# Kernel tuning notes

Hardware: AMD Instinct MI355X
Metric: run time of the kernel (lower is better)

Reference implementation:

```python
import jax, jax.numpy as jnp
import numpy as np

B, D, C = 16384, 2048, 1000  # batch, in_features (feature dim), out_features (classes)
INIT_SCALE = 10.0
EPS = 1e-12


def setup_inputs() -> dict:
    key = jax.random.key(0)
    k1, k2 = jax.random.split(key)
    x = jax.random.normal(k1, (B, D), dtype=jnp.float32)
    weights = jax.random.normal(k2, (C, D), dtype=jnp.float32)  # prototypes
    scales = jnp.ones((1,), dtype=jnp.float32) * INIT_SCALE
    return {"x": x, "weights": weights, "scales": scales}


def reference(x, weights, scales):
    # Pairwise Euclidean distance between features [B,D] and prototypes [C,D]
    x2 = jnp.sum(x * x, axis=-1, keepdims=True)            # [B,1]
    w2 = jnp.sum(weights * weights, axis=-1)               # [C]
    cross = jnp.einsum('bd,cd->bc', x, weights)            # [B,C]
    d2 = jnp.maximum(x2 + w2[None, :] - 2.0 * cross, EPS)  # clamp for sqrt stability
    distances = jnp.sqrt(d2)                               # [B,C]
    logits = -scales * distances  # dml forward: -self.learn(distances)
    return logits
```

## Files before the change

### kernel.cpp

```cpp
#include <hip/hip_runtime.h>
#include <hip/hip_bf16.h>
#include <stdint.h>

#define B_ROWS 16384
#define D_K    2048
#define C_COLS 1000
#define C_PAD  1024
#define EPS_D2 1e-12f

#define BM 256
#define BN 256
#define BK 32
#define NT (D_K / BK)
#define BUF_BYTES 32768
#define NBUF 4

typedef __attribute__((ext_vector_type(8))) short bf16x8;
typedef __attribute__((ext_vector_type(4))) float f32x4;

__device__ __forceinline__ void async16(void* lds, const void* g) {
    __builtin_amdgcn_global_load_lds(
        (const __attribute__((address_space(1))) unsigned int*)g,
        (__attribute__((address_space(3))) unsigned int*)lds,
        16, 0, 0);
}

__device__ __forceinline__ uint2 pack_bf16x4(float4 v) {
    union { __hip_bfloat162 h; uint32_t u; } a, b;
    a.h = __float22bfloat162_rn(make_float2(v.x, v.y));
    b.h = __float22bfloat162_rn(make_float2(v.z, v.w));
    uint2 r; r.x = a.u; r.y = b.u; return r;
}

__global__ __launch_bounds__(256) void prep_all(
    const float* __restrict__ x, const float* __restrict__ w,
    __hip_bfloat16* __restrict__ xb, __hip_bfloat16* __restrict__ wb,
    float* __restrict__ x2, float* __restrict__ w2) {
    const int t = threadIdx.x;
    const int wave = t >> 6;
    const int lane = t & 63;
    const int row = blockIdx.x * 4 + wave;

    const float* src;
    uint4* dst;
    float* norm_out;
    bool valid;
    if (row < B_ROWS) {
        src = x + (size_t)row * D_K;
        dst = (uint4*)(xb + (size_t)row * D_K);
        norm_out = x2 + row;
        valid = true;
    } else {
        int c = row - B_ROWS;
        src = w + (size_t)c * D_K;
        dst = (uint4*)(wb + (size_t)c * D_K);
        norm_out = w2 + c;
        valid = (c < C_COLS);
    }

    float4 v[8];
    if (valid) {
        const float4* s4 = (const float4*)src;
        #pragma unroll
        for (int i = 0; i < 4; i++) {
            v[2 * i]     = s4[2 * lane + 128 * i];
            v[2 * i + 1] = s4[2 * lane + 1 + 128 * i];
        }
    } else {
        #pragma unroll
        for (int i = 0; i < 8; i++) v[i] = make_float4(0.f, 0.f, 0.f, 0.f);
    }

    float ss = 0.f;
    #pragma unroll
    for (int i = 0; i < 8; i++)
        ss += v[i].x * v[i].x + v[i].y * v[i].y + v[i].z * v[i].z + v[i].w * v[i].w;

    #pragma unroll
    for (int i = 0; i < 4; i++) {
        uint2 a = pack_bf16x4(v[2 * i]);
        uint2 b = pack_bf16x4(v[2 * i + 1]);
        uint4 p; p.x = a.x; p.y = a.y; p.z = b.x; p.w = b.y;
        dst[lane + 64 * i] = p;
    }

    #pragma unroll
    for (int off = 32; off > 0; off >>= 1) ss += __shfl_down(ss, off, 64);
    if (lane == 0 && valid) *norm_out = ss;
}

__global__ __launch_bounds__(512, 2) void dml_gemm(
    const __hip_bfloat16* __restrict__ A,
    const __hip_bfloat16* __restrict__ Bm,
    const float* __restrict__ x2, const float* __restrict__ w2,
    const float* __restrict__ scales, float* __restrict__ out)
{
    __shared__ __align__(16) char smem[NBUF * BUF_BYTES];

    const int tid  = threadIdx.x;
    const int wave = tid >> 6;
    const int lane = tid & 63;
    const int wm = wave >> 2;
    const int wn = wave & 3;

    const int id  = blockIdx.x;
    const int xcd = id & 7;
    const int j5  = id >> 3;
    const int m0  = (xcd * 8 + (j5 & 7)) * BM;
    const int n0  = (j5 >> 3) * BN;

    const int L0 = tid, L1 = tid + 512;
    const int r0 = L0 >> 2, g0 = (L0 & 3) ^ ((r0 >> 1) & 3);
    const int r1 = L1 >> 2, g1 = (L1 & 3) ^ ((r1 >> 1) & 3);
    const __hip_bfloat16* pA0 = A  + (size_t)(m0 + r0) * D_K + g0 * 8;
    const __hip_bfloat16* pA1 = A  + (size_t)(m0 + r1) * D_K + g1 * 8;
    const __hip_bfloat16* pB0 = Bm + (size_t)(n0 + r0) * D_K + g0 * 8;
    const __hip_bfloat16* pB1 = Bm + (size_t)(n0 + r1) * D_K + g1 * 8;
    char* ldA0 = smem + L0 * 16;
    char* ldA1 = smem + L1 * 16;
    char* ldB0 = smem + 16384 + L0 * 16;
    char* ldB1 = smem + 16384 + L1 * 16;

    const int fr = lane & 15;
    const int fq = lane >> 4;
    const int ksw = (fq ^ ((fr >> 1) & 3)) * 16;
    const char* fA = smem + (wm * 128 + fr) * 64 + ksw;
    const char* fB = smem + 16384 + (wn * 64 + fr) * 64 + ksw;

    f32x4 acc[8][4] = {};

    #pragma unroll
    for (int tgt = 0; tgt < 3; ++tgt) {
        const int sbo = tgt * BUF_BYTES;
        async16(ldA0 + sbo, pA0 + tgt * BK);
        async16(ldA1 + sbo, pA1 + tgt * BK);
        async16(ldB0 + sbo, pB0 + tgt * BK);
        async16(ldB1 + sbo, pB1 + tgt * BK);
    }
    asm volatile("s_waitcnt vmcnt(8)" ::: "memory");
    __builtin_amdgcn_s_barrier();
    __builtin_amdgcn_sched_barrier(0);

    #pragma unroll 1
    for (int t = 0; t < NT; ++t) {
        const int bo  = (t & 3) * BUF_BYTES;
        const int tgt = t + 3;
        const bool do_stage = (tgt < NT);
        const int sbo = (tgt & 3) * BUF_BYTES;

        if (do_stage) {
            async16(ldA0 + sbo, pA0 + tgt * BK);
            async16(ldA1 + sbo, pA1 + tgt * BK);
        }
        bf16x8 b[4], a[4];
        #pragma unroll
        for (int q = 0; q < 4; ++q) b[q] = *(const bf16x8*)(fB + bo + q * 1024);
        #pragma unroll
        for (int i = 0; i < 4; ++i) a[i] = *(const bf16x8*)(fA + bo + i * 1024);
        __builtin_amdgcn_s_setprio(1);
        #pragma unroll
        for (int i = 0; i < 4; ++i)
            #pragma unroll
            for (int q = 0; q < 4; ++q)
                acc[i][q] = __builtin_amdgcn_mfma_f32_16x16x32_bf16(a[i], b[q], acc[i][q], 0, 0, 0);
        __builtin_amdgcn_s_setprio(0);

        if (do_stage) {
            async16(ldB0 + sbo, pB0 + tgt * BK);
            async16(ldB1 + sbo, pB1 + tgt * BK);
        }
        #pragma unroll
        for (int i = 0; i < 4; ++i) a[i] = *(const bf16x8*)(fA + bo + (4 + i) * 1024);
        __builtin_amdgcn_s_setprio(1);
        #pragma unroll
        for (int i = 0; i < 4; ++i)
            #pragma unroll
            for (int q = 0; q < 4; ++q)
                acc[4 + i][q] = __builtin_amdgcn_mfma_f32_16x16x32_bf16(a[i], b[q], acc[4 + i][q], 0, 0, 0);
        __builtin_amdgcn_s_setprio(0);

        if (t < NT - 3)      asm volatile("s_waitcnt vmcnt(8)" ::: "memory");
        else if (t == NT - 3) asm volatile("s_waitcnt vmcnt(4)" ::: "memory");
        else if (t == NT - 2) asm volatile("s_waitcnt vmcnt(0)" ::: "memory");
        if (t < NT - 1) {
            __builtin_amdgcn_s_barrier();
            __builtin_amdgcn_sched_barrier(0);
        }
    }

    const float s = scales[0];
    const int colb = n0 + wn * 64 + fr;
    const int rowb = m0 + wm * 128 + fq * 4;

    float w2v[4];
    #pragma unroll
    for (int q = 0; q < 4; ++q) w2v[q] = w2[colb + q * 16];

    #pragma unroll
    for (int i = 0; i < 8; ++i) {
        float x2v[4];
        #pragma unroll
        for (int r = 0; r < 4; ++r) x2v[r] = x2[rowb + i * 16 + r];
        #pragma unroll
        for (int q = 0; q < 4; ++q) {
            if (colb + q * 16 < C_COLS) {
                float* orow = out + (size_t)(rowb + i * 16) * C_COLS + colb + q * 16;
                #pragma unroll
                for (int r = 0; r < 4; ++r) {
                    float d2 = x2v[r] + w2v[q] - 2.0f * acc[i][q][r];
                    d2 = fmaxf(d2, EPS_D2);
                    orow[(size_t)r * C_COLS] = -s * __builtin_sqrtf(d2);
                }
            }
        }
    }
}

extern "C" void kernel_launch(void* const* d_in, const int* in_sizes, int n_in,
                              void* d_out, int out_size, void* d_ws, size_t ws_size,
                              hipStream_t stream) {
    const float* x      = (const float*)d_in[0];
    const float* w      = (const float*)d_in[1];
    const float* scales = (const float*)d_in[2];
    float* out = (float*)d_out;

    char* ws = (char*)d_ws;
    __hip_bfloat16* xb = (__hip_bfloat16*)ws;
    __hip_bfloat16* wb = (__hip_bfloat16*)(ws + (size_t)B_ROWS * D_K * 2);
    float* x2 = (float*)(ws + (size_t)B_ROWS * D_K * 2 + (size_t)C_PAD * D_K * 2);
    float* w2 = x2 + B_ROWS;

    prep_all<<<dim3((B_ROWS + C_PAD) / 4), dim3(256), 0, stream>>>(x, w, xb, wb, x2, w2);
    dml_gemm<<<dim3((B_ROWS / BM) * (C_PAD / BN)), dim3(512), 0, stream>>>(xb, wb, x2, w2, scales, out);
}
```

Measured before the change: 286.7 us.

## Software-pipeline LDS fragment loads one k-tile ahead of MFMA compute

The main loop now reads the next k-tile's A and B fragments from LDS into registers while the second half of the current tile's MFMAs run, instead of loading fragments right before they are used. The barrier moves to mid-iteration, and the global-to-LDS async loads for a tile are issued together after it, with vmcnt waits adjusted to match. The goal is to hide LDS read latency behind matrix-core work. The cost is extra live VGPRs for the double-buffered fragments, which could cause spills or lower occupancy under the 512-thread, 2-block launch bounds.

```diff
diff --git a/kernel.cpp b/kernel.cpp
--- a/kernel.cpp
+++ b/kernel.cpp
@@ -141,50 +141,65 @@
     __builtin_amdgcn_s_barrier();
     __builtin_amdgcn_sched_barrier(0);
 
+    bf16x8 aA[4], bb[4], a1[4];
+    #pragma unroll
+    for (int i = 0; i < 4; ++i) aA[i] = *(const bf16x8*)(fA + i * 1024);
+    #pragma unroll
+    for (int q = 0; q < 4; ++q) bb[q] = *(const bf16x8*)(fB + q * 1024);
+    #pragma unroll
+    for (int i = 0; i < 4; ++i) a1[i] = *(const bf16x8*)(fA + (4 + i) * 1024);
+
     #pragma unroll 1
     for (int t = 0; t < NT; ++t) {
-        const int bo  = (t & 3) * BUF_BYTES;
+        const int bo1 = ((t + 1) & 3) * BUF_BYTES;
         const int tgt = t + 3;
-        const bool do_stage = (tgt < NT);
-        const int sbo = (tgt & 3) * BUF_BYTES;
-
-        if (do_stage) {
-            async16(ldA0 + sbo, pA0 + tgt * BK);
-            async16(ldA1 + sbo, pA1 + tgt * BK);
-        }
-        bf16x8 b[4], a[4];
-        #pragma unroll
-        for (int q = 0; q < 4; ++q) b[q] = *(const bf16x8*)(fB + bo + q * 1024);
-        #pragma unroll
-        for (int i = 0; i < 4; ++i) a[i] = *(const bf16x8*)(fA + bo + i * 1024);
+
         __builtin_amdgcn_s_setprio(1);
         #pragma unroll
         for (int i = 0; i < 4; ++i)
             #pragma unroll
             for (int q = 0; q < 4; ++q)
-                acc[i][q] = __builtin_amdgcn_mfma_f32_16x16x32_bf16(a[i], b[q], acc[i][q], 0, 0, 0);
+                acc[i][q] = __builtin_amdgcn_mfma_f32_16x16x32_bf16(aA[i], bb[q], acc[i][q], 0, 0, 0);
         __builtin_amdgcn_s_setprio(0);
 
-        if (do_stage) {
-            async16(ldB0 + sbo, pB0 + tgt * BK);
-            async16(ldB1 + sbo, pB1 + tgt * BK);
-        }
-        #pragma unroll
-        for (int i = 0; i < 4; ++i) a[i] = *(const bf16x8*)(fA + bo + (4 + i) * 1024);
-        __builtin_amdgcn_s_setprio(1);
-        #pragma unroll
-        for (int i = 0; i < 4; ++i)
-            #pragma unroll
-            for (int q = 0; q < 4; ++q)
-                acc[4 + i][q] = __builtin_amdgcn_mfma_f32_16x16x32_bf16(a[i], b[q], acc[4 + i][q], 0, 0, 0);
-        __builtin_amdgcn_s_setprio(0);
-
-        if (t < NT - 3)      asm volatile("s_waitcnt vmcnt(8)" ::: "memory");
-        else if (t == NT - 3) asm volatile("s_waitcnt vmcnt(4)" ::: "memory");
+        if (t < NT - 2)       asm volatile("s_waitcnt vmcnt(4)" ::: "memory");
         else if (t == NT - 2) asm volatile("s_waitcnt vmcnt(0)" ::: "memory");
         if (t < NT - 1) {
             __builtin_amdgcn_s_barrier();
             __builtin_amdgcn_sched_barrier(0);
+        }
+
+        if (tgt < NT) {
+            const int sbo = (tgt & 3) * BUF_BYTES;
+            async16(ldA0 + sbo, pA0 + tgt * BK);
+            async16(ldA1 + sbo, pA1 + tgt * BK);
+            async16(ldB0 + sbo, pB0 + tgt * BK);
+            async16(ldB1 + sbo, pB1 + tgt * BK);
+        }
+
+        bf16x8 aN[4], bN[4];
+        if (t + 1 < NT) {
+            #pragma unroll
+            for (int i = 0; i < 4; ++i) aN[i] = *(const bf16x8*)(fA + bo1 + i * 1024);
+            #pragma unroll
+            for (int q = 0; q < 4; ++q) bN[q] = *(const bf16x8*)(fB + bo1 + q * 1024);
+        }
+
+        __builtin_amdgcn_s_setprio(1);
+        #pragma unroll
+        for (int i = 0; i < 4; ++i)
+            #pragma unroll
+            for (int q = 0; q < 4; ++q)
+                acc[4 + i][q] = __builtin_amdgcn_mfma_f32_16x16x32_bf16(a1[i], bb[q], acc[4 + i][q], 0, 0, 0);
+        __builtin_amdgcn_s_setprio(0);
+
+        if (t + 1 < NT) {
+            #pragma unroll
+            for (int i = 0; i < 4; ++i) a1[i] = *(const bf16x8*)(fA + bo1 + (4 + i) * 1024);
+            #pragma unroll
+            for (int i = 0; i < 4; ++i) aA[i] = aN[i];
+            #pragma unroll
+            for (int q = 0; q < 4; ++q) bb[q] = bN[q];
         }
     }
 
```

After: 287.9 us. No clear change (+0.4%).

## Restructure GEMM main loop into fine-grained 8-phase pipelined schedule

Applied to the files above, without the earlier changes.

Replaces the 4-buffer BK=32 loop with a 128-K-wide iteration split into eight phases over two 64-K buffers of two 32-K halves each. Async global-to-LDS loads are interleaved with LDS reads and MFMA blocks, with a barrier before and after each MFMA block. The aim is to spread memory issue evenly across compute and keep MFMAs fed. The cost is many more barriers per K step, a larger 128KB LDS footprint, and a fragile hand-tuned vmcnt accounting.

```diff
diff --git a/kernel.cpp b/kernel.cpp
--- a/kernel.cpp
+++ b/kernel.cpp
@@ -10,10 +10,7 @@
 
 #define BM 256
 #define BN 256
-#define BK 32
-#define NT (D_K / BK)
-#define BUF_BYTES 32768
-#define NBUF 4
+#define NIT (D_K / 128)
 
 typedef __attribute__((ext_vector_type(8))) short bf16x8;
 typedef __attribute__((ext_vector_type(4))) float f32x4;
@@ -89,13 +86,51 @@
     if (lane == 0 && valid) *norm_out = ss;
 }
 
+#define SLOT(buf, kh) ((buf) * 65536 + (kh) * 16384)
+
+#define SA(buf, kh, t) { \
+    async16(lA0 + SLOT(buf, kh), gA0 + (t) * 64 + (kh) * 32); \
+    async16(lA1 + SLOT(buf, kh), gA1 + (t) * 64 + (kh) * 32); }
+
+#define SB(buf, kh, t) { \
+    async16(lB0 + SLOT(buf, kh), gB0 + (t) * 64 + (kh) * 32); \
+    async16(lB1 + SLOT(buf, kh), gB1 + (t) * 64 + (kh) * 32); }
+
+#define RD_B(buf, kh) { \
+    b[0] = *(const bf16x8*)(fB + SLOT(buf, kh)); \
+    b[1] = *(const bf16x8*)(fB + SLOT(buf, kh) + 1024); \
+    b[2] = *(const bf16x8*)(fB + SLOT(buf, kh) + 2048); \
+    b[3] = *(const bf16x8*)(fB + SLOT(buf, kh) + 3072); }
+
+#define RD_A(buf, kh, mh) { \
+    a[0] = *(const bf16x8*)(fA + SLOT(buf, kh) + (mh) * 4096); \
+    a[1] = *(const bf16x8*)(fA + SLOT(buf, kh) + (mh) * 4096 + 1024); \
+    a[2] = *(const bf16x8*)(fA + SLOT(buf, kh) + (mh) * 4096 + 2048); \
+    a[3] = *(const bf16x8*)(fA + SLOT(buf, kh) + (mh) * 4096 + 3072); }
+
+#define SYNC_IN { \
+    __builtin_amdgcn_s_barrier(); \
+    asm volatile("s_waitcnt lgkmcnt(0)" ::: "memory"); \
+    __builtin_amdgcn_sched_barrier(0); }
+
+#define MFMA_BLK(base) { \
+    __builtin_amdgcn_s_setprio(1); \
+    _Pragma("unroll") \
+    for (int i = 0; i < 4; ++i) \
+        _Pragma("unroll") \
+        for (int q = 0; q < 4; ++q) \
+            acc[(base) + i][q] = __builtin_amdgcn_mfma_f32_16x16x32_bf16(a[i], b[q], acc[(base) + i][q], 0, 0, 0); \
+    __builtin_amdgcn_s_setprio(0); }
+
+#define SYNC_OUT __builtin_amdgcn_s_barrier();
+
 __global__ __launch_bounds__(512, 2) void dml_gemm(
     const __hip_bfloat16* __restrict__ A,
     const __hip_bfloat16* __restrict__ Bm,
     const float* __restrict__ x2, const float* __restrict__ w2,
     const float* __restrict__ scales, float* __restrict__ out)
 {
-    __shared__ __align__(16) char smem[NBUF * BUF_BYTES];
+    __shared__ __align__(16) char smem[131072];
 
     const int tid  = threadIdx.x;
     const int wave = tid >> 6;
@@ -112,80 +147,71 @@
     const int L0 = tid, L1 = tid + 512;
     const int r0 = L0 >> 2, g0 = (L0 & 3) ^ ((r0 >> 1) & 3);
     const int r1 = L1 >> 2, g1 = (L1 & 3) ^ ((r1 >> 1) & 3);
-    const __hip_bfloat16* pA0 = A  + (size_t)(m0 + r0) * D_K + g0 * 8;
-    const __hip_bfloat16* pA1 = A  + (size_t)(m0 + r1) * D_K + g1 * 8;
-    const __hip_bfloat16* pB0 = Bm + (size_t)(n0 + r0) * D_K + g0 * 8;
-    const __hip_bfloat16* pB1 = Bm + (size_t)(n0 + r1) * D_K + g1 * 8;
-    char* ldA0 = smem + L0 * 16;
-    char* ldA1 = smem + L1 * 16;
-    char* ldB0 = smem + 16384 + L0 * 16;
-    char* ldB1 = smem + 16384 + L1 * 16;
+    const __hip_bfloat16* gA0 = A  + (size_t)(m0 + r0) * D_K + g0 * 8;
+    const __hip_bfloat16* gA1 = A  + (size_t)(m0 + r1) * D_K + g1 * 8;
+    const __hip_bfloat16* gB0 = Bm + (size_t)(n0 + r0) * D_K + g0 * 8;
+    const __hip_bfloat16* gB1 = Bm + (size_t)(n0 + r1) * D_K + g1 * 8;
+    char* lA0 = smem + L0 * 16;
+    char* lA1 = smem + L1 * 16;
+    char* lB0 = smem + 32768 + L0 * 16;
+    char* lB1 = smem + 32768 + L1 * 16;
 
     const int fr = lane & 15;
     const int fq = lane >> 4;
-    const int ksw = (fq ^ ((fr >> 1) & 3)) * 16;
-    const char* fA = smem + (wm * 128 + fr) * 64 + ksw;
-    const char* fB = smem + 16384 + (wn * 64 + fr) * 64 + ksw;
+    const int swz = (fq ^ ((fr >> 1) & 3)) * 16;
+    const char* fA = smem + (wm * 128 + fr) * 64 + swz;
+    const char* fB = smem + 32768 + (wn * 64 + fr) * 64 + swz;
 
     f32x4 acc[8][4] = {};
 
-    #pragma unroll
-    for (int tgt = 0; tgt < 3; ++tgt) {
-        const int sbo = tgt * BUF_BYTES;
-        async16(ldA0 + sbo, pA0 + tgt * BK);
-        async16(ldA1 + sbo, pA1 + tgt * BK);
-        async16(ldB0 + sbo, pB0 + tgt * BK);
-        async16(ldB1 + sbo, pB1 + tgt * BK);
-    }
-    asm volatile("s_waitcnt vmcnt(8)" ::: "memory");
+    SA(0, 0, 0); SB(0, 0, 0); SA(0, 1, 0); SB(0, 1, 0);
+    SA(1, 0, 1); SB(1, 0, 1); SB(1, 1, 1);
+    asm volatile("s_waitcnt vmcnt(0)" ::: "memory");
     __builtin_amdgcn_s_barrier();
     __builtin_amdgcn_sched_barrier(0);
 
     #pragma unroll 1
-    for (int t = 0; t < NT; ++t) {
-        const int bo  = (t & 3) * BUF_BYTES;
-        const int tgt = t + 3;
-        const bool do_stage = (tgt < NT);
-        const int sbo = (tgt & 3) * BUF_BYTES;
-
-        if (do_stage) {
-            async16(ldA0 + sbo, pA0 + tgt * BK);
-            async16(ldA1 + sbo, pA1 + tgt * BK);
-        }
-        bf16x8 b[4], a[4];
-        #pragma unroll
-        for (int q = 0; q < 4; ++q) b[q] = *(const bf16x8*)(fB + bo + q * 1024);
-        #pragma unroll
-        for (int i = 0; i < 4; ++i) a[i] = *(const bf16x8*)(fA + bo + i * 1024);
-        __builtin_amdgcn_s_setprio(1);
-        #pragma unroll
-        for (int i = 0; i < 4; ++i)
-            #pragma unroll
-            for (int q = 0; q < 4; ++q)
-                acc[i][q] = __builtin_amdgcn_mfma_f32_16x16x32_bf16(a[i], b[q], acc[i][q], 0, 0, 0);
-        __builtin_amdgcn_s_setprio(0);
-
-        if (do_stage) {
-            async16(ldB0 + sbo, pB0 + tgt * BK);
-            async16(ldB1 + sbo, pB1 + tgt * BK);
-        }
-        #pragma unroll
-        for (int i = 0; i < 4; ++i) a[i] = *(const bf16x8*)(fA + bo + (4 + i) * 1024);
-        __builtin_amdgcn_s_setprio(1);
-        #pragma unroll
-        for (int i = 0; i < 4; ++i)
-            #pragma unroll
-            for (int q = 0; q < 4; ++q)
-                acc[4 + i][q] = __builtin_amdgcn_mfma_f32_16x16x32_bf16(a[i], b[q], acc[4 + i][q], 0, 0, 0);
-        __builtin_amdgcn_s_setprio(0);
-
-        if (t < NT - 3)      asm volatile("s_waitcnt vmcnt(8)" ::: "memory");
-        else if (t == NT - 3) asm volatile("s_waitcnt vmcnt(4)" ::: "memory");
-        else if (t == NT - 2) asm volatile("s_waitcnt vmcnt(0)" ::: "memory");
-        if (t < NT - 1) {
-            __builtin_amdgcn_s_barrier();
-            __builtin_amdgcn_sched_barrier(0);
-        }
+    for (int it = 0; it < NIT; ++it) {
+        const int t2 = 2 * it + 2, t3 = 2 * it + 3;
+        const bool st = (it < NIT - 1);
+        bf16x8 a[4], b[4];
+
+        RD_B(0, 0); RD_A(0, 0, 0);
+        SA(1, 1, 2 * it + 1);
+        SYNC_IN; MFMA_BLK(0); SYNC_OUT;
+
+        RD_A(0, 0, 1);
+        if (st) SB(0, 0, t2);
+        SYNC_IN; MFMA_BLK(4); SYNC_OUT;
+
+        RD_B(0, 1); RD_A(0, 1, 0);
+        if (st) SA(0, 0, t2);
+        SYNC_IN; MFMA_BLK(0); SYNC_OUT;
+
+        RD_A(0, 1, 1);
+        if (st) SB(0, 1, t2);
+        SYNC_IN; MFMA_BLK(4);
+        if (st) asm volatile("s_waitcnt vmcnt(6)" ::: "memory");
+        else    asm volatile("s_waitcnt vmcnt(0)" ::: "memory");
+        SYNC_OUT;
+
+        RD_B(1, 0); RD_A(1, 0, 0);
+        if (st) SA(0, 1, t2);
+        SYNC_IN; MFMA_BLK(0); SYNC_OUT;
+
+        RD_A(1, 0, 1);
+        if (st) SB(1, 0, t3);
+        SYNC_IN; MFMA_BLK(4); SYNC_OUT;
+
+        RD_B(1, 1); RD_A(1, 1, 0);
+        if (st) SA(1, 0, t3);
+        SYNC_IN; MFMA_BLK(0); SYNC_OUT;
+
+        RD_A(1, 1, 1);
+        if (st) SB(1, 1, t3);
+        SYNC_IN; MFMA_BLK(4);
+        if (st) asm volatile("s_waitcnt vmcnt(6)" ::: "memory");
+        SYNC_OUT;
     }
 
     const float s = scales[0];
```

New measurement: 289.6 us. Within noise of the previous version (+1.0%).

## Compute row norms of x inside GEMM from bf16 LDS tiles

Applied to the files above, without the earlier changes.

Removes the x squared-norm computation from the prep kernel and instead accumulates it inside the GEMM main loop from the bf16 A fragments already loaded into registers. Work is split so each of the four N-waves handles one K-tile in four, and the partials are reduced with shuffles and shared memory before the epilogue. This drops one global read per row and some prep ALU work, but adds VALU work in the hot loop and computes the norm from bf16-rounded values rather than fp32. That rounding changes numerics, though it arguably matches the bf16 cross term more closely.

```diff
diff --git a/kernel.cpp b/kernel.cpp
--- a/kernel.cpp
+++ b/kernel.cpp
@@ -30,6 +30,17 @@
     a.h = __float22bfloat162_rn(make_float2(v.x, v.y));
     b.h = __float22bfloat162_rn(make_float2(v.z, v.w));
     uint2 r; r.x = a.u; r.y = b.u; return r;
+}
+
+__device__ __forceinline__ void acc_sq(float* p, bf16x8 v) {
+    union { bf16x8 s; uint32_t u[4]; } c; c.s = v;
+    #pragma unroll
+    for (int j = 0; j < 4; ++j) {
+        float lo = __uint_as_float(c.u[j] << 16);
+        float hi = __uint_as_float(c.u[j] & 0xffff0000u);
+        *p += lo * lo;
+        *p += hi * hi;
+    }
 }
 
 __global__ __launch_bounds__(256) void prep_all(
@@ -40,15 +51,15 @@
     const int wave = t >> 6;
     const int lane = t & 63;
     const int row = blockIdx.x * 4 + wave;
+    const bool isx = (row < B_ROWS);
 
     const float* src;
     uint4* dst;
-    float* norm_out;
+    float* norm_out = nullptr;
     bool valid;
-    if (row < B_ROWS) {
+    if (isx) {
         src = x + (size_t)row * D_K;
         dst = (uint4*)(xb + (size_t)row * D_K);
-        norm_out = x2 + row;
         valid = true;
     } else {
         int c = row - B_ROWS;
@@ -71,11 +82,6 @@
         for (int i = 0; i < 8; i++) v[i] = make_float4(0.f, 0.f, 0.f, 0.f);
     }
 
-    float ss = 0.f;
-    #pragma unroll
-    for (int i = 0; i < 8; i++)
-        ss += v[i].x * v[i].x + v[i].y * v[i].y + v[i].z * v[i].z + v[i].w * v[i].w;
-
     #pragma unroll
     for (int i = 0; i < 4; i++) {
         uint2 a = pack_bf16x4(v[2 * i]);
@@ -84,9 +90,15 @@
         dst[lane + 64 * i] = p;
     }
 
-    #pragma unroll
-    for (int off = 32; off > 0; off >>= 1) ss += __shfl_down(ss, off, 64);
-    if (lane == 0 && valid) *norm_out = ss;
+    if (!isx) {
+        float ss = 0.f;
+        #pragma unroll
+        for (int i = 0; i < 8; i++)
+            ss += v[i].x * v[i].x + v[i].y * v[i].y + v[i].z * v[i].z + v[i].w * v[i].w;
+        #pragma unroll
+        for (int off = 32; off > 0; off >>= 1) ss += __shfl_down(ss, off, 64);
+        if (lane == 0 && valid) *norm_out = ss;
+    }
 }
 
 __global__ __launch_bounds__(512, 2) void dml_gemm(
@@ -121,13 +133,14 @@
     char* ldB0 = smem + 16384 + L0 * 16;
     char* ldB1 = smem + 16384 + L1 * 16;
 
-    const int fr = lane & 15;
-    const int fq = lane >> 4;
-    const int ksw = (fq ^ ((fr >> 1) & 3)) * 16;
-    const char* fA = smem + (wm * 128 + fr) * 64 + ksw;
-    const char* fB = smem + 16384 + (wn * 64 + fr) * 64 + ksw;
+    const int fr  = lane & 15;
+    const int fq  = lane >> 4;
+    const int fsw = (fr >> 1) & 3;
+    const char* fA = smem + (wm * 128 + fr) * 64 + (fq ^ fsw) * 16;
+    const char* fB = smem + 16384 + (wn * 64 + fr) * 64 + (fq ^ fsw) * 16;
 
     f32x4 acc[8][4] = {};
+    float p2[8] = {0.f, 0.f, 0.f, 0.f, 0.f, 0.f, 0.f, 0.f};
 
     #pragma unroll
     for (int tgt = 0; tgt < 3; ++tgt) {
@@ -147,6 +160,7 @@
         const int tgt = t + 3;
         const bool do_stage = (tgt < NT);
         const int sbo = (tgt & 3) * BUF_BYTES;
+        const bool sqact = ((t & 3) == wn);
 
         if (do_stage) {
             async16(ldA0 + sbo, pA0 + tgt * BK);
@@ -157,6 +171,10 @@
         for (int q = 0; q < 4; ++q) b[q] = *(const bf16x8*)(fB + bo + q * 1024);
         #pragma unroll
         for (int i = 0; i < 4; ++i) a[i] = *(const bf16x8*)(fA + bo + i * 1024);
+        if (sqact) {
+            #pragma unroll
+            for (int i = 0; i < 4; ++i) acc_sq(&p2[i], a[i]);
+        }
         __builtin_amdgcn_s_setprio(1);
         #pragma unroll
         for (int i = 0; i < 4; ++i)
@@ -171,6 +189,10 @@
         }
         #pragma unroll
         for (int i = 0; i < 4; ++i) a[i] = *(const bf16x8*)(fA + bo + (4 + i) * 1024);
+        if (sqact) {
+            #pragma unroll
+            for (int i = 0; i < 4; ++i) acc_sq(&p2[4 + i], a[i]);
+        }
         __builtin_amdgcn_s_setprio(1);
         #pragma unroll
         for (int i = 0; i < 4; ++i)
@@ -179,7 +201,7 @@
                 acc[4 + i][q] = __builtin_amdgcn_mfma_f32_16x16x32_bf16(a[i], b[q], acc[4 + i][q], 0, 0, 0);
         __builtin_amdgcn_s_setprio(0);
 
-        if (t < NT - 3)      asm volatile("s_waitcnt vmcnt(8)" ::: "memory");
+        if (t < NT - 3)       asm volatile("s_waitcnt vmcnt(8)" ::: "memory");
         else if (t == NT - 3) asm volatile("s_waitcnt vmcnt(4)" ::: "memory");
         else if (t == NT - 2) asm volatile("s_waitcnt vmcnt(0)" ::: "memory");
         if (t < NT - 1) {
@@ -188,6 +210,19 @@
         }
     }
 
+    #pragma unroll
+    for (int mi = 0; mi < 8; ++mi) {
+        p2[mi] += __shfl_xor(p2[mi], 16, 64);
+        p2[mi] += __shfl_xor(p2[mi], 32, 64);
+    }
+    float* smx = (float*)smem;
+    if (fq == 0) {
+        #pragma unroll
+        for (int mi = 0; mi < 8; ++mi)
+            smx[wn * 256 + wm * 128 + mi * 16 + fr] = p2[mi];
+    }
+    __syncthreads();
+
     const float s = scales[0];
     const int colb = n0 + wn * 64 + fr;
     const int rowb = m0 + wm * 128 + fq * 4;
@@ -200,7 +235,10 @@
     for (int i = 0; i < 8; ++i) {
         float x2v[4];
         #pragma unroll
-        for (int r = 0; r < 4; ++r) x2v[r] = x2[rowb + i * 16 + r];
+        for (int r = 0; r < 4; ++r) {
+            const int rl = wm * 128 + i * 16 + fq * 4 + r;
+            x2v[r] = smx[rl] + smx[256 + rl] + smx[512 + rl] + smx[768 + rl];
+        }
         #pragma unroll
         for (int q = 0; q < 4; ++q) {
             if (colb + q * 16 < C_COLS) {
```

Result: slower. 314.8 us (+9.8%).
